# Kernel tuning notes

Hardware: AMD Instinct MI355X
Metric: run time of the kernel (lower is better)

## Reference

```python
import jax, jax.numpy as jnp
import numpy as np

N_ENT = 40000
N_REL2 = 500      # num_rel * 2
E_DIR = 200000
E_2HOP = 50000
D_IN = 128        # entity/relation init dim
D_EMB = 256       # embed_dim
N_HEADS = 4
N_HID = D_EMB // N_HEADS  # 64
LRELU_ALPHA = 0.2
BN_EPS = 1e-5


def setup_inputs() -> dict:
    key = jax.random.key(0)
    ks = jax.random.split(key, 13)
    s = 0.1  # weight init scale
    return {
        "edge_index": jax.random.randint(ks[0], (2, E_DIR), 0, N_ENT),
        "edge_type": jax.random.randint(ks[1], (E_DIR,), 0, N_REL2),
        "indices_2hop": jax.random.randint(ks[2], (E_2HOP, 4), 0, N_REL2),
        "init_embed": jax.random.normal(ks[3], (N_ENT, D_IN), jnp.float32) * s,
        "init_rel": jax.random.normal(ks[4], (N_REL2, D_IN), jnp.float32) * s,
        "W_heads": jax.random.normal(ks[5], (N_HEADS, 2 * D_IN + D_IN, N_HID), jnp.float32) * s,
        "a_heads": jax.random.normal(ks[6], (N_HEADS, N_HID, 1), jnp.float32) * s,
        "gat_W": jax.random.normal(ks[7], (D_IN, D_EMB), jnp.float32) * s,
        "out_W": jax.random.normal(ks[8], (2 * D_EMB + D_EMB, D_EMB), jnp.float32) * s,
        "out_a": jax.random.normal(ks[9], (D_EMB, 1), jnp.float32) * s,
        "W_entities": jax.random.normal(ks[10], (D_IN, D_EMB), jnp.float32) * s,
        "bn_gamma": jnp.ones((D_EMB,), jnp.float32),
        "bn_beta": jnp.zeros((D_EMB,), jnp.float32),
    }


def segment_softmax(logits, idx, num_seg):
    # sparse softmax grouped by idx (PyG-style): subtract per-segment max, exp, normalize
    m = jax.ops.segment_max(logits, idx, num_segments=num_seg)
    e = jnp.exp(logits - m[idx])
    s = jax.ops.segment_sum(e, idx, num_segments=num_seg)
    return e / (s[idx] + 1e-16)


def reference(edge_index, edge_type, indices_2hop, init_embed, init_rel,
              W_heads, a_heads, gat_W, out_W, out_a, W_entities, bn_gamma, bn_beta):
    n = init_embed.shape[0]
    # build full edge list: flipped direct edges + 2-hop edges
    edge_nhop = jnp.stack([indices_2hop[:, 3], indices_2hop[:, 0]])  # [2, E2]
    ei = jnp.concatenate([edge_index[::-1], edge_nhop], axis=1)      # [2, Etot]
    row, col = ei[0], ei[1]
    t0, t1 = indices_2hop[:, 1], indices_2hop[:, 2]

    # first-layer edge relation embeddings
    edge_embed = jnp.concatenate([init_rel[edge_type], init_rel[t0] + init_rel[t1]], axis=0)
    feat = jnp.concatenate([init_embed[row], init_embed[col], edge_embed], axis=1)  # [Etot, 3*D_IN]

    def head(W, a):
        eh = feat @ W                                     # [Etot, N_HID]
        logit = jax.nn.leaky_relu((eh @ a)[:, 0], LRELU_ALPHA)
        alpha = segment_softmax(logit, row, n)
        agg = jax.ops.segment_sum(alpha[:, None] * eh, row, num_segments=n)
        return jax.nn.elu(agg)                            # concat=True -> elu

    x = jax.vmap(head)(W_heads, a_heads)                  # [H, N, N_HID]
    x = jnp.transpose(x, (1, 0, 2)).reshape(n, -1)        # [N, H*N_HID]

    r = init_rel @ gat_W                                  # [R2, D_EMB]
    edge_embed2 = jnp.concatenate([r[edge_type], r[t0] + r[t1]], axis=0)
    feat2 = jnp.concatenate([x[row], x[col], edge_embed2], axis=1)  # [Etot, 3*D_EMB]
    eh2 = feat2 @ out_W                                   # [Etot, D_EMB]
    logit2 = jax.nn.leaky_relu((eh2 @ out_a)[:, 0], LRELU_ALPHA)
    alpha2 = segment_softmax(logit2, row, n)
    out = jax.ops.segment_sum(alpha2[:, None] * eh2, row, num_segments=n)
    x = jax.nn.elu(out)                                   # elu applied in GAT.forward

    x = x + init_embed @ W_entities
    # BatchNorm1d (training-mode batch stats, biased variance)
    mu = jnp.mean(x, axis=0)
    var = jnp.var(x, axis=0)
    x = (x - mu) / jnp.sqrt(var + BN_EPS) * bn_gamma + bn_beta
    return x, r
```

## Files before the change

kernel.cpp:

```cpp
#include <hip/hip_runtime.h>
#include <hip/hip_bf16.h>
#include <math.h>

#define N_ENT 40000
#define N_REL 500
#define E_DIR 200000
#define E_2HOP 50000
#define E_TOT 250000
#define D_IN 128
#define D_EMB 256
#define LRELU 0.2f
#define BN_EPS 1e-5f
#define NB_SCAN 157
#define NB_EDGE 977
#define N_HEAVY 500
#define DEG_SPLIT 32

typedef __hip_bfloat16 bf16;
typedef __attribute__((ext_vector_type(8))) short short8;
typedef __attribute__((ext_vector_type(4))) float float4v;

__device__ __forceinline__ float b2f(bf16 v){ return __bfloat162float(v); }
__device__ __forceinline__ float bitsf(unsigned int u){ return __builtin_bit_cast(float, u); }
__device__ __forceinline__ unsigned short bbits(float v){ return __builtin_bit_cast(unsigned short, __float2bfloat16(v)); }

__device__ __forceinline__ int e_row(int e, const int* ei, const int* i2){
  return (e < E_DIR) ? ei[E_DIR + e] : i2[(e - E_DIR)*4 + 3];
}

__global__ void prep_hist(const float* __restrict__ Wh, const float* __restrict__ ow,
                          const float* __restrict__ we, const float* __restrict__ emb,
                          bf16* __restrict__ WAp, bf16* __restrict__ WBp, bf16* __restrict__ WEp,
                          bf16* __restrict__ OWp0, bf16* __restrict__ OWp1, float* __restrict__ WC,
                          bf16* __restrict__ embb,
                          const int* __restrict__ ei, const int* __restrict__ i2, int* __restrict__ cnt){
  const int HS = 384*64;
  int b = blockIdx.x, tid = threadIdx.x;
  if (b < NB_EDGE){
    int e = b*256 + tid;
    if (e < E_TOT) atomicAdd(&cnt[e_row(e, ei, i2)], 1);
    return;
  }
  b -= NB_EDGE;
  if (b >= 240){
    int i = (b - 240)*256 + tid;
    embb[i] = __float2bfloat16(emb[i]);
    return;
  }
  if (b < 112){
    int seg, base;
    if      (b < 16){ seg = 0; base = 0; }
    else if (b < 32){ seg = 1; base = 16; }
    else if (b < 48){ seg = 2; base = 32; }
    else if (b < 80){ seg = 3; base = 48; }
    else            { seg = 4; base = 80; }
    int idx = (b - base)*256 + tid;
    int lane = idx & 63, nt = (idx >> 6) & 15, kc = idx >> 10;
    int quad = lane >> 4, l16 = lane & 15;
    int col = nt*16 + l16;
    int kbase = kc*32 + quad*8;
    bf16* dst = (seg==0?WAp : seg==1?WBp : seg==2?WEp : seg==3?OWp0 : OWp1) + (size_t)idx*8;
    #pragma unroll
    for (int j = 0; j < 8; j++){
      int k = kbase + j;
      float v;
      if      (seg == 0) v = Wh[(col>>6)*HS + k*64 + (col&63)];
      else if (seg == 1) v = Wh[(col>>6)*HS + (k+128)*64 + (col&63)];
      else if (seg == 2) v = we[(size_t)k*256 + col];
      else if (seg == 3) v = ow[(size_t)k*256 + col];
      else               v = ow[(size_t)(k+256)*256 + col];
      dst[j] = __float2bfloat16(v);
    }
  } else {
    int idx = (b - 112)*256 + tid;
    int k = idx >> 8, col = idx & 255;
    WC[idx] = Wh[(col>>6)*HS + (k+256)*64 + (col&63)];
  }
}

__global__ void scan_bsum(const int* __restrict__ cnt, int* __restrict__ bsum){
  int i = blockIdx.x*256 + threadIdx.x;
  int v = (i < N_ENT) ? cnt[i] : 0;
  int lane = threadIdx.x & 63, w = threadIdx.x >> 6;
  int s = v;
  #pragma unroll
  for (int o = 32; o >= 1; o >>= 1) s += __shfl_xor(s, o, 64);
  __shared__ int ws[4];
  if (lane == 0) ws[w] = s;
  __syncthreads();
  if (threadIdx.x == 0) bsum[blockIdx.x] = ws[0]+ws[1]+ws[2]+ws[3];
}

__global__ __launch_bounds__(256) void scan_final2(const int* __restrict__ cnt,
    const int* __restrict__ bsum, int* __restrict__ off){
  __shared__ int boffs[NB_SCAN];
  __shared__ int ws4[4];
  __shared__ int ws2[4];
  __shared__ int totals;
  int t = threadIdx.x;
  int lane = t & 63, w = t >> 6;
  {
    int v = (t < NB_SCAN) ? bsum[t] : 0;
    int s = v;
    #pragma unroll
    for (int o = 1; o < 64; o <<= 1){ int n = __shfl_up(s, o, 64); if (lane >= o) s += n; }
    if (lane == 63) ws4[w] = s;
    __syncthreads();
    int add = 0;
    for (int k = 0; k < w; k++) add += ws4[k];
    int incl = s + add;
    if (t < NB_SCAN) boffs[t] = incl - v;
    if (t == NB_SCAN-1) totals = incl;
  }
  __syncthreads();
  int i = blockIdx.x*256 + t;
  int v = (i < N_ENT) ? cnt[i] : 0;
  int s = v;
  #pragma unroll
  for (int o = 1; o < 64; o <<= 1){ int n = __shfl_up(s, o, 64); if (lane >= o) s += n; }
  if (lane == 63) ws2[w] = s;
  __syncthreads();
  int add = boffs[blockIdx.x];
  for (int k = 0; k < w; k++) add += ws2[k];
  if (i < N_ENT) off[i] = add + s - v;
  if (blockIdx.x == 0 && t == 0) off[N_ENT] = totals;
}

__device__ __forceinline__ void mfma_panel(const short* __restrict__ A,
    const short* __restrict__ Bp, bf16* __restrict__ C, int K,
    const float* __restrict__ avec, float* __restrict__ Sout, int dmode, int bx){
  int w = threadIdx.x >> 6, lane = threadIdx.x & 63;
  int quad = lane >> 4, l16 = lane & 15;
  int rm = bx*64 + w*16;
  int arow = rm + l16;
  float4v acc[16];
  #pragma unroll
  for (int nt = 0; nt < 16; nt++) acc[nt] = (float4v){0.f,0.f,0.f,0.f};
  int nkc = K >> 5;
  const short8* Ap = (const short8*)(A + (size_t)arow*K);
  const short8* Bv = (const short8*)Bp;
  short8 a_cur = Ap[quad];
  for (int kc = 0; kc < nkc; kc++){
    int kn = (kc + 1 < nkc) ? kc + 1 : kc;
    short8 a_nxt = Ap[kn*4 + quad];
    const short8* bp = Bv + (size_t)kc*16*64 + lane;
    short8 b[8];
    #pragma unroll
    for (int nt = 0; nt < 8; nt++) b[nt] = bp[(size_t)nt*64];
    #pragma unroll
    for (int nt = 0; nt < 8; nt++)
      acc[nt] = __builtin_amdgcn_mfma_f32_16x16x32_bf16(a_cur, b[nt], acc[nt], 0, 0, 0);
    #pragma unroll
    for (int nt = 0; nt < 8; nt++) b[nt] = bp[(size_t)(nt+8)*64];
    #pragma unroll
    for (int nt = 0; nt < 8; nt++)
      acc[nt+8] = __builtin_amdgcn_mfma_f32_16x16x32_bf16(a_cur, b[nt], acc[nt+8], 0, 0, 0);
    a_cur = a_nxt;
  }
  #pragma unroll
  for (int nt = 0; nt < 16; nt++){
    #pragma unroll
    for (int r = 0; r < 4; r++){
      int row = quad*4 + r;
      C[(size_t)(rm + row)*256 + nt*16 + l16] = __float2bfloat16(acc[nt][r]);
    }
  }
  if (Sout){
    if (dmode == 0){
      #pragma unroll
      for (int h = 0; h < 4; h++){
        float pr[4] = {0.f,0.f,0.f,0.f};
        #pragma unroll
        for (int ntl = 0; ntl < 4; ntl++){
          int nt = h*4 + ntl;
          float av = avec[nt*16 + l16];
          #pragma unroll
          for (int r = 0; r < 4; r++) pr[r] += acc[nt][r]*av;
        }
        #pragma unroll
        for (int m = 8; m >= 1; m >>= 1)
          #pragma unroll
          for (int r = 0; r < 4; r++) pr[r] += __shfl_xor(pr[r], m, 64);
        if (l16 == 0){
          #pragma unroll
          for (int r = 0; r < 4; r++) Sout[(rm + quad*4 + r)*4 + h] = pr[r];
        }
      }
    } else {
      float pr[4] = {0.f,0.f,0.f,0.f};
      #pragma unroll
      for (int nt = 0; nt < 16; nt++){
        float av = avec[nt*16 + l16];
        #pragma unroll
        for (int r = 0; r < 4; r++) pr[r] += acc[nt][r]*av;
      }
      #pragma unroll
      for (int m = 8; m >= 1; m >>= 1)
        #pragma unroll
        for (int r = 0; r < 4; r++) pr[r] += __shfl_xor(pr[r], m, 64);
      if (l16 == 0){
        #pragma unroll
        for (int r = 0; r < 4; r++) Sout[rm + quad*4 + r] = pr[r];
      }
    }
  }
}

__device__ __forceinline__ void gemm64_body(const float* __restrict__ A,
    const float* __restrict__ B, float* __restrict__ C, bf16* __restrict__ Cb,
    int M, int K, const float* __restrict__ av, float* __restrict__ So, int mode,
    int bxx, int byy){
  const int N = 256;
  __shared__ float As[16][65];
  __shared__ float Bs[16][65];
  int bm = bxx * 64, bn = byy * 64;
  int tid = threadIdx.x;
  int tx = tid & 15, ty = tid >> 4;
  float acc[4][4] = {};
  for (int k0 = 0; k0 < K; k0 += 16){
    #pragma unroll
    for (int j = 0; j < 4; j++){
      int idx = tid + j*256;
      int m = idx >> 4, kk = idx & 15;
      int gm = bm + m;
      float v = 0.f;
      if (gm < M) v = A[(size_t)gm*K + k0 + kk];
      As[kk][m] = v;
    }
    #pragma unroll
    for (int j = 0; j < 4; j++){
      int idx = tid + j*256;
      int kk = idx >> 6, n = idx & 63;
      Bs[kk][n] = B[(size_t)(k0+kk)*N + bn + n];
    }
    __syncthreads();
    #pragma unroll
    for (int kk = 0; kk < 16; kk++){
      float a[4], b[4];
      #pragma unroll
      for (int i = 0; i < 4; i++) a[i] = As[kk][ty*4+i];
      #pragma unroll
      for (int j = 0; j < 4; j++) b[j] = Bs[kk][tx*4+j];
      #pragma unroll
      for (int i = 0; i < 4; i++)
        #pragma unroll
        for (int j = 0; j < 4; j++) acc[i][j] += a[i]*b[j];
    }
    __syncthreads();
  }
  if (Cb){
    #pragma unroll
    for (int i = 0; i < 4; i++){
      int gm = bm + ty*4 + i;
      if (gm >= M) continue;
      #pragma unroll
      for (int j = 0; j < 4; j++)
        Cb[(size_t)gm*N + bn + tx*4 + j] = __float2bfloat16(acc[i][j]);
    }
  } else {
    #pragma unroll
    for (int i = 0; i < 4; i++){
      int gm = bm + ty*4 + i;
      if (gm >= M) continue;
      #pragma unroll
      for (int j = 0; j < 4; j++)
        C[(size_t)gm*N + bn + tx*4 + j] = acc[i][j];
    }
  }
  if (mode != 2){
    float pr[4];
    #pragma unroll
    for (int i = 0; i < 4; i++){
      float p = 0.f;
      #pragma unroll
      for (int j = 0; j < 4; j++) p += acc[i][j]*av[bn + tx*4 + j];
      pr[i] = p;
    }
    #pragma unroll
    for (int m = 8; m >= 1; m >>= 1)
      #pragma unroll
      for (int i = 0; i < 4; i++) pr[i] += __shfl_xor(pr[i], m, 64);
    if (tx == 0){
      #pragma unroll
      for (int i = 0; i < 4; i++){
        int gm = bm + ty*4 + i;
        if (gm < M){
          if (mode == 0) So[gm*4 + byy] = pr[i];
          else atomicAdd(&So[gm], pr[i]);
        }
      }
    }
  }
}

__device__ __forceinline__ void scatter_body(const int* __restrict__ ei, const int* __restrict__ et,
    const int* __restrict__ i2, const int* __restrict__ off,
    int* __restrict__ cur, int4* __restrict__ EIDX, int blk){
  int e = blk*256 + threadIdx.x;
  if (e >= E_TOT) return;
  int r = e_row(e, ei, i2);
  int p = atomicAdd(&cur[r], 1);
  int d = off[r] + p;
  int4 v;
  if (e < E_DIR){ v.x = ei[e]; v.y = et[e]; v.z = -1; }
  else { int q = (e - E_DIR)*4; v.x = i2[q]; v.y = i2[q+1]; v.z = i2[q+2]; }
  v.w = r;
  EIDX[d] = v;
}

__global__ __launch_bounds__(256) void mega1(
    const short* __restrict__ embb, const short* __restrict__ WAp, const short* __restrict__ WBp,
    const short* __restrict__ WEp, bf16* __restrict__ P1, bf16* __restrict__ P2, bf16* __restrict__ EP,
    const float* __restrict__ ah, float* __restrict__ S1, float* __restrict__ S2,
    const float* __restrict__ rel, const float* __restrict__ WC, const float* __restrict__ gw,
    float* __restrict__ RF, float* __restrict__ SRm, bf16* __restrict__ PRb,
    const int* __restrict__ ei, const int* __restrict__ et, const int* __restrict__ i2,
    const int* __restrict__ off, int* __restrict__ cur, int4* __restrict__ EIDX, int useEP){
  int y = blockIdx.y, x = blockIdx.x;
  if (x < 625){
    if (y == 2 && !useEP) return;
    const short* B = y==0 ? WAp : (y==1 ? WBp : WEp);
    bf16* C = y==0 ? P1 : (y==1 ? P2 : EP);
    float* S = y==0 ? S1 : (y==1 ? S2 : nullptr);
    mfma_panel(embb, B, C, 128, ah, S, 0, x);
    return;
  }
  int r = x - 625;
  if (y == 0){
    if (r < 64){
      int z = r >> 5, rr = r & 31, by = rr >> 3, bx = rr & 7;
      if (z == 0) gemm64_body(rel, WC, nullptr, PRb, N_REL, 128, ah, SRm, 0, bx, by);
      else        gemm64_body(rel, gw, RF, nullptr, N_REL, 128, nullptr, nullptr, 2, bx, by);
    }
  } else if (y == 1){
    if (r < NB_EDGE) scatter_body(ei, et, i2, off, cur, EIDX, r);
  }
}

__global__ __launch_bounds__(256) void mega2(
    const short* __restrict__ X1s, const short* __restrict__ OWp0, const short* __restrict__ OWp1,
    bf16* __restrict__ Q1, bf16* __restrict__ Q2, const float* __restrict__ oa,
    float* __restrict__ S1B, float* __restrict__ S2B,
    const float* __restrict__ RF, const float* __restrict__ owB, float* __restrict__ SRB,
    bf16* __restrict__ QRb){
  int y = blockIdx.y, x = blockIdx.x;
  if (x < 625){
    mfma_panel(X1s, y==0 ? OWp0 : OWp1, y==0 ? Q1 : Q2, 256, oa, y==0 ? S1B : S2B, 1, x);
    return;
  }
  int r = x - 625;
  if (y == 0 && r < 32){
    int by = r >> 3, bx = r & 7;
    gemm64_body(RF, owB, nullptr, QRb, N_REL, 256, oa, SRB, 1, bx, by);
  }
}

__global__ void gemm64_acc(const float* __restrict__ A, const float* __restrict__ B,
                           float* __restrict__ C, int M, int K){
  const int N = 256;
  __shared__ float As[16][65];
  __shared__ float Bs[16][65];
  int bm = blockIdx.x * 64, bn = blockIdx.y * 64;
  int tid = threadIdx.x;
  int tx = tid & 15, ty = tid >> 4;
  float acc[4][4] = {};
  for (int k0 = 0; k0 < K; k0 += 16){
    #pragma unroll
    for (int j = 0; j < 4; j++){
      int idx = tid + j*256;
      int m = idx >> 4, kk = idx & 15;
      int gm = bm + m;
      float v = 0.f;
      if (gm < M) v = A[(size_t)gm*K + k0 + kk];
      As[kk][m] = v;
    }
    #pragma unroll
    for (int j = 0; j < 4; j++){
      int idx = tid + j*256;
      int kk = idx >> 6, n = idx & 63;
      Bs[kk][n] = B[(size_t)(k0+kk)*N + bn + n];
    }
    __syncthreads();
    #pragma unroll
    for (int kk = 0; kk < 16; kk++){
      float a[4], b[4];
      #pragma unroll
      for (int i = 0; i < 4; i++) a[i] = As[kk][ty*4+i];
      #pragma unroll
      for (int j = 0; j < 4; j++) b[j] = Bs[kk][tx*4+j];
      #pragma unroll
      for (int i = 0; i < 4; i++)
        #pragma unroll
        for (int j = 0; j < 4; j++) acc[i][j] += a[i]*b[j];
    }
    __syncthreads();
  }
  #pragma unroll
  for (int i = 0; i < 4; i++){
    int gm = bm + ty*4 + i;
    if (gm >= M) continue;
    #pragma unroll
    for (int j = 0; j < 4; j++){
      size_t o = (size_t)gm*N + bn + tx*4 + j;
      C[o] += acc[i][j];
    }
  }
}

__global__ __launch_bounds__(256) void sm1f(const int* __restrict__ off, const int4* __restrict__ EIDX,
    const float* __restrict__ s1, const float* __restrict__ s2, const float* __restrict__ sR,
    float* __restrict__ L1, float* __restrict__ AS1, float* __restrict__ IV1){
  if (blockIdx.x < N_HEAVY){
    int i = blockIdx.x;
    int st = off[i], en = off[i+1];
    if (en - st <= DEG_SPLIT) return;
    int h = threadIdx.x >> 6, lane = threadIdx.x & 63;
    float* Lh = L1 + (size_t)h*E_TOT;
    float si = s1[i*4 + h];
    float mx = -1e30f;
    for (int t = st + lane; t < en; t += 64){
      int4 e = EIDX[t];
      float v = si + s2[e.x*4+h] + sR[e.y*4+h];
      if (e.z >= 0) v += sR[e.z*4+h];
      v = (v >= 0.f) ? v : LRELU*v;
      Lh[t] = v;
      mx = fmaxf(mx, v);
    }
    #pragma unroll
    for (int o = 32; o >= 1; o >>= 1) mx = fmaxf(mx, __shfl_xor(mx, o, 64));
    float sm = 0.f;
    for (int t = st + lane; t < en; t += 64){
      float ev = __expf(Lh[t] - mx); Lh[t] = ev; sm += ev;
    }
    #pragma unroll
    for (int o = 32; o >= 1; o >>= 1) sm += __shfl_xor(sm, o, 64);
    float inv = 1.f/(sm + 1e-16f);
    if (lane == 0){ AS1[i*4+h] = sm*inv; IV1[i*4+h] = inv; }
    return;
  }
  int wid = threadIdx.x >> 6, lane = threadIdx.x & 63;
  int i = (blockIdx.x - N_HEAVY)*4 + wid;
  if (i >= N_ENT) return;
  int st = off[i], en = off[i+1];
  if (i < N_HEAVY && en - st > DEG_SPLIT) return;
  int hf = lane >> 4, l16 = lane & 15;
  float* Lh = L1 + (size_t)hf*E_TOT;
  float si = s1[i*4 + hf];
  if (en - st > 2*16){
    float mx = -1e30f;
    for (int t = st + l16; t < en; t += 16){
      int4 e = EIDX[t];
      float v = si + s2[e.x*4+hf] + sR[e.y*4+hf];
      if (e.z >= 0) v += sR[e.z*4+hf];
      v = (v >= 0.f) ? v : LRELU*v;
      Lh[t] = v; mx = fmaxf(mx, v);
    }
    #pragma unroll
    for (int o = 8; o >= 1; o >>= 1) mx = fmaxf(mx, __shfl_xor(mx, o, 64));
    float sm = 0.f;
    for (int t = st + l16; t < en; t += 16){
      float ev = __expf(Lh[t] - mx); Lh[t] = ev; sm += ev;
    }
    #pragma unroll
    for (int o = 8; o >= 1; o >>= 1) sm += __shfl_xor(sm, o, 64);
    float inv = 1.f/(sm + 1e-16f);
    if (l16 == 0){ AS1[i*4+hf] = sm*inv; IV1[i*4+hf] = inv; }
    return;
  }
  int t0 = st + l16, t1 = t0 + 16;
  float v0 = -1e30f, v1 = -1e30f;
  if (t0 < en){
    int4 e = EIDX[t0];
    float v = si + s2[e.x*4+hf] + sR[e.y*4+hf];
    if (e.z >= 0) v += sR[e.z*4+hf];
    v0 = (v >= 0.f) ? v : LRELU*v;
  }
  if (t1 < en){
    int4 e = EIDX[t1];
    float v = si + s2[e.x*4+hf] + sR[e.y*4+hf];
    if (e.z >= 0) v += sR[e.z*4+hf];
    v1 = (v >= 0.f) ? v : LRELU*v;
  }
  float mx = fmaxf(v0, v1);
  #pragma unroll
  for (int o = 8; o >= 1; o >>= 1) mx = fmaxf(mx, __shfl_xor(mx, o, 64));
  float sm = 0.f;
  if (t0 < en){ float ev = __expf(v0 - mx); Lh[t0] = ev; sm += ev; }
  if (t1 < en){ float ev = __expf(v1 - mx); Lh[t1] = ev; sm += ev; }
  #pragma unroll
  for (int o = 8; o >= 1; o >>= 1) sm += __shfl_xor(sm, o, 64);
  float inv = 1.f/(sm + 1e-16f);
  if (l16 == 0){ AS1[i*4+hf] = sm*inv; IV1[i*4+hf] = inv; }
}

__global__ __launch_bounds__(256) void sm2f(const int* __restrict__ off, const int4* __restrict__ EIDX,
    const float* __restrict__ s1, const float* __restrict__ s2, const float* __restrict__ sR,
    float* __restrict__ L2, float* __restrict__ AS2, float* __restrict__ IV2){
  __shared__ float wsm[4], wss[4];
  if (blockIdx.x < N_HEAVY){
    int i = blockIdx.x;
    int st = off[i], en = off[i+1];
    if (en - st <= DEG_SPLIT) return;
    int tid = threadIdx.x, w = tid >> 6, lane = tid & 63;
    float si = s1[i];
    float mx = -1e30f;
    for (int t = st + tid; t < en; t += 256){
// ... 321 lines not shown
  }
  float a0=0,a1=0,a2=0,a3=0;
  int t = st;
  int n4 = st + ((en - st) & ~3);
  for (; t < n4; t += 4){
    int4 e[4]; float wv[4]; uint2 u[4]; uint2 rr[4];
    #pragma unroll
    for (int k = 0; k < 4; k++){ e[k] = EIDX[t+k]; wv[k] = W2[t+k]; }
    #pragma unroll
    for (int k = 0; k < 4; k++){
      u[k] = *(const uint2*)(Q2 + (size_t)e[k].x*256 + f0);
      rr[k] = *(const uint2*)(QRm + (size_t)e[k].y*256 + f0);
    }
    float rf[4][4];
    #pragma unroll
    for (int k = 0; k < 4; k++){ UNPK(rr[k], rf[k][0], rf[k][1], rf[k][2], rf[k][3]) }
    #pragma unroll
    for (int k = 0; k < 4; k++){
      if (e[k].z >= 0){
        uint2 s = *(const uint2*)(QRm + (size_t)e[k].z*256 + f0);
        float s0,s1,s2,s3; UNPK(s, s0,s1,s2,s3)
        rf[k][0] += s0; rf[k][1] += s1; rf[k][2] += s2; rf[k][3] += s3;
      }
    }
    #pragma unroll
    for (int k = 0; k < 4; k++){
      a0 += wv[k]*(bitsf(u[k].x << 16) + rf[k][0]);
      a1 += wv[k]*(bitsf(u[k].x & 0xffff0000u) + rf[k][1]);
      a2 += wv[k]*(bitsf(u[k].y << 16) + rf[k][2]);
      a3 += wv[k]*(bitsf(u[k].y & 0xffff0000u) + rf[k][3]);
    }
  }
  for (; t < en; t++){
    float w = W2[t];
    int4 e = EIDX[t];
    uint2 u = *(const uint2*)(Q2 + (size_t)e.x*256 + f0);
    uint2 rr = *(const uint2*)(QRm + (size_t)e.y*256 + f0);
    float r0,r1,r2,r3; UNPK(rr, r0,r1,r2,r3)
    if (e.z >= 0){
      uint2 s = *(const uint2*)(QRm + (size_t)e.z*256 + f0);
      float s0,s1,s2,s3; UNPK(s, s0,s1,s2,s3)
      r0 += s0; r1 += s1; r2 += s2; r3 += s3;
    }
    a0 += w*(bitsf(u.x << 16) + r0);
    a1 += w*(bitsf(u.x & 0xffff0000u) + r1);
    a2 += w*(bitsf(u.y << 16) + r2);
    a3 += w*(bitsf(u.y & 0xffff0000u) + r3);
  }
  float iv = IV2[i];
  a0 *= iv; a1 *= iv; a2 *= iv; a3 *= iv;
  float as = AS2[i];
  uint2 uq = *(const uint2*)(Q1 + ob);
  a0 += as*bitsf(uq.x << 16);
  a1 += as*bitsf(uq.x & 0xffff0000u);
  a2 += as*bitsf(uq.y << 16);
  a3 += as*bitsf(uq.y & 0xffff0000u);
  a0 = ((a0 > 0.f) ? a0 : __expf(a0)-1.f) + ep0;
  a1 = ((a1 > 0.f) ? a1 : __expf(a1)-1.f) + ep1;
  a2 = ((a2 > 0.f) ? a2 : __expf(a2)-1.f) + ep2;
  a3 = ((a3 > 0.f) ? a3 : __expf(a3)-1.f) + ep3;
  *(float4*)(X2 + ob) = (float4){a0, a1, a2, a3};
}

__global__ void bn_reduce(const float* __restrict__ X, float* __restrict__ sums, float* __restrict__ sq){
  int ch = threadIdx.x;
  float s = 0.f, q = 0.f;
  for (int r = blockIdx.x; r < N_ENT; r += gridDim.x){
    float v = X[(size_t)r*256 + ch];
    s += v; q += v*v;
  }
  atomicAdd(&sums[ch], s);
  atomicAdd(&sq[ch], q);
}

__global__ void bn_final_r(float* __restrict__ X, const float* __restrict__ sums, const float* __restrict__ sq,
                           const float* __restrict__ gamma, const float* __restrict__ beta,
                           const float* __restrict__ RF, float* __restrict__ out_r){
  int b = blockIdx.x;
  if (b < 40000){
    int idx = b*256 + threadIdx.x;
    int ch = idx & 255;
    const float invn = 1.f/(float)N_ENT;
    float mean = sums[ch] * invn;
    float var  = fmaxf(sq[ch] * invn - mean*mean, 0.f);
    X[idx] = (X[idx] - mean) * rsqrtf(var + BN_EPS) * gamma[ch] + beta[ch];
  } else {
    int idx = (b - 40000)*256 + threadIdx.x;
    out_r[idx] = RF[idx];
  }
}

extern "C" void kernel_launch(void* const* d_in, const int* in_sizes, int n_in,
                              void* d_out, int out_size, void* d_ws, size_t ws_size,
                              hipStream_t stream){
  const int*   ei  = (const int*)d_in[0];
  const int*   et  = (const int*)d_in[1];
  const int*   i2  = (const int*)d_in[2];
  const float* emb = (const float*)d_in[3];
  const float* rel = (const float*)d_in[4];
  const float* Wh  = (const float*)d_in[5];
  const float* ah  = (const float*)d_in[6];
  const float* gw  = (const float*)d_in[7];
  const float* ow  = (const float*)d_in[8];
  const float* oa  = (const float*)d_in[9];
  const float* we  = (const float*)d_in[10];
  const float* gma = (const float*)d_in[11];
  const float* bta = (const float*)d_in[12];
  float* out = (float*)d_out;

  char* ws = (char*)d_ws;
  size_t o = 0;
  auto alloc = [&](size_t bytes)->char*{
    char* p = ws + o; o = (o + bytes + 255) & ~(size_t)255; return p;
  };
  bf16*  P1  = (bf16*)alloc(20480000);
  bf16*  P2  = (bf16*)alloc(20480000);
  bf16*  PRb = (bf16*)alloc(256000);
  bf16*  QRb = (bf16*)alloc(256000);
  float* RF  = (float*)alloc(512000);
  float* WC  = (float*)alloc(131072);
  bf16*  WAp = (bf16*)alloc(65536);
  bf16*  WBp = (bf16*)alloc(65536);
  bf16*  WEp = (bf16*)alloc(65536);
  bf16*  OWp0= (bf16*)alloc(131072);
  bf16*  OWp1= (bf16*)alloc(131072);
  float* S1  = (float*)alloc(640000);
  float* S2  = (float*)alloc(640000);
  float* SRm = (float*)alloc(8192);
  float* S1B = (float*)alloc(160000);
  float* S2B = (float*)alloc(160000);
  int*   CNT = (int*)alloc(160000);
  int*   CUR = (int*)alloc(160000);
  float* SRB = (float*)alloc(2048);
  float* BNS = (float*)alloc(1024);
  float* BNQ = (float*)alloc(1024);
  int*   OFF = (int*)alloc(160016);
  int*   BSUM= (int*)alloc(1024);
  int4*  EIDX= (int4*)alloc(4000000);
  float* L1  = (float*)alloc(4000000);
  float* L2  = (float*)alloc(1000000);
  float* AS1 = (float*)alloc(640000);
  float* AS2 = (float*)alloc(160000);
  float* IV1 = (float*)alloc(640000);
  float* IV2 = (float*)alloc(160000);
  size_t base_end = o;
  bool useEP = (ws_size >= base_end + 20480256 + 512);
  bf16* EP = nullptr;
  if (useEP) EP = (bf16*)alloc(20480000);
  bf16* X1b  = (bf16*)out;
  bf16* embb = (bf16*)((char*)out + 20480000);
  float* X2 = out;
  (void)in_sizes; (void)n_in; (void)out_size;

  hipMemsetAsync(CNT, 0, 324096, stream);

  prep_hist<<<NB_EDGE + 20240, 256, 0, stream>>>(Wh, ow, we, emb,
      WAp, WBp, WEp, OWp0, OWp1, WC, embb, ei, i2, CNT);

  scan_bsum<<<NB_SCAN, 256, 0, stream>>>(CNT, BSUM);
  scan_final2<<<NB_SCAN, 256, 0, stream>>>(CNT, BSUM, OFF);

  mega1<<<dim3(625 + NB_EDGE, 3), 256, 0, stream>>>(
      (const short*)embb, (const short*)WAp, (const short*)WBp, (const short*)WEp,
      P1, P2, EP, ah, S1, S2,
      rel, WC, gw, RF, SRm, PRb,
      ei, et, i2, OFF, CUR, EIDX, useEP ? 1 : 0);

  sm1f<<<N_HEAVY + N_ENT/4, 256, 0, stream>>>(OFF, EIDX, S1, S2, SRm, L1, AS1, IV1);
  agg1<<<N_HEAVY + N_ENT/4, 256, 0, stream>>>(OFF, EIDX, L1, AS1, IV1, P1, P2, PRb, X1b);

  mega2<<<dim3(625 + 32, 2), 256, 0, stream>>>(
      (const short*)X1b, (const short*)OWp0, (const short*)OWp1,
      P1, P2, oa, S1B, S2B, RF, ow + 131072, SRB, QRb);

  sm2f<<<N_HEAVY + N_ENT/4, 256, 0, stream>>>(OFF, EIDX, S1B, S2B, SRB, L2, AS2, IV2);
  agg2<<<N_HEAVY + N_ENT/4, 256, 0, stream>>>(OFF, EIDX, L2, AS2, IV2, P1, P2, QRb, EP, X2);

  if (!useEP)
    gemm64_acc<<<dim3((N_ENT+63)/64, 4), 256, 0, stream>>>(emb, we, X2, N_ENT, 128);

  bn_reduce<<<1024, 256, 0, stream>>>(X2, BNS, BNQ);
  bn_final_r<<<40500, 256, 0, stream>>>(X2, BNS, BNQ, gma, bta, RF, out + (size_t)N_ENT*256);
}
```

Before: 404.6 us.

## Split MFMA panels into column halves with atomic score accumulation

Each MFMA panel block now computes only half of the 256 output columns, so there are twice as many blocks and half as many accumulator registers per thread, with launch bounds raised to allow more waves per CU. The per-row attention dot products in the second layer are now combined across the two halves with atomicAdd, which requires zeroing the score buffers; the memset is widened to start at S1B. Shared memory is moved to an explicit buffer so the combined kernels use one allocation. The aim is better occupancy and latency hiding in the projection GEMMs, at the cost of reloading A rows twice and adding atomics.

```diff
diff --git a/kernel.cpp b/kernel.cpp
--- a/kernel.cpp
+++ b/kernel.cpp
@@ -128,54 +128,54 @@
 
 __device__ __forceinline__ void mfma_panel(const short* __restrict__ A,
     const short* __restrict__ Bp, bf16* __restrict__ C, int K,
-    const float* __restrict__ avec, float* __restrict__ Sout, int dmode, int bx){
+    const float* __restrict__ avec, float* __restrict__ Sout, int dmode,
+    int bx, int half){
   int w = threadIdx.x >> 6, lane = threadIdx.x & 63;
   int quad = lane >> 4, l16 = lane & 15;
   int rm = bx*64 + w*16;
   int arow = rm + l16;
-  float4v acc[16];
+  float4v acc[8];
   #pragma unroll
-  for (int nt = 0; nt < 16; nt++) acc[nt] = (float4v){0.f,0.f,0.f,0.f};
+  for (int nt = 0; nt < 8; nt++) acc[nt] = (float4v){0.f,0.f,0.f,0.f};
   int nkc = K >> 5;
   const short8* Ap = (const short8*)(A + (size_t)arow*K);
-  const short8* Bv = (const short8*)Bp;
+  const short8* Bv = (const short8*)Bp + half*512 + lane;
   short8 a_cur = Ap[quad];
   for (int kc = 0; kc < nkc; kc++){
     int kn = (kc + 1 < nkc) ? kc + 1 : kc;
     short8 a_nxt = Ap[kn*4 + quad];
-    const short8* bp = Bv + (size_t)kc*16*64 + lane;
-    short8 b[8];
-    #pragma unroll
-    for (int nt = 0; nt < 8; nt++) b[nt] = bp[(size_t)nt*64];
-    #pragma unroll
-    for (int nt = 0; nt < 8; nt++)
+    const short8* bp = Bv + (size_t)kc*1024;
+    short8 b[4];
+    #pragma unroll
+    for (int nt = 0; nt < 4; nt++) b[nt] = bp[nt*64];
+    #pragma unroll
+    for (int nt = 0; nt < 4; nt++)
       acc[nt] = __builtin_amdgcn_mfma_f32_16x16x32_bf16(a_cur, b[nt], acc[nt], 0, 0, 0);
     #pragma unroll
-    for (int nt = 0; nt < 8; nt++) b[nt] = bp[(size_t)(nt+8)*64];
-    #pragma unroll
-    for (int nt = 0; nt < 8; nt++)
-      acc[nt+8] = __builtin_amdgcn_mfma_f32_16x16x32_bf16(a_cur, b[nt], acc[nt+8], 0, 0, 0);
+    for (int nt = 0; nt < 4; nt++) b[nt] = bp[(nt+4)*64];
+    #pragma unroll
+    for (int nt = 0; nt < 4; nt++)
+      acc[nt+4] = __builtin_amdgcn_mfma_f32_16x16x32_bf16(a_cur, b[nt], acc[nt+4], 0, 0, 0);
     a_cur = a_nxt;
   }
   #pragma unroll
-  for (int nt = 0; nt < 16; nt++){
-    #pragma unroll
-    for (int r = 0; r < 4; r++){
-      int row = quad*4 + r;
-      C[(size_t)(rm + row)*256 + nt*16 + l16] = __float2bfloat16(acc[nt][r]);
-    }
+  for (int nt = 0; nt < 8; nt++){
+    int col = (half*8 + nt)*16 + l16;
+    #pragma unroll
+    for (int r = 0; r < 4; r++)
+      C[(size_t)(rm + quad*4 + r)*256 + col] = __float2bfloat16(acc[nt][r]);
   }
   if (Sout){
     if (dmode == 0){
       #pragma unroll
-      for (int h = 0; h < 4; h++){
+      for (int hl = 0; hl < 2; hl++){
         float pr[4] = {0.f,0.f,0.f,0.f};
         #pragma unroll
         for (int ntl = 0; ntl < 4; ntl++){
-          int nt = h*4 + ntl;
-          float av = avec[nt*16 + l16];
+          int ln = hl*4 + ntl;
+          float av = avec[(half*8 + ln)*16 + l16];
           #pragma unroll
-          for (int r = 0; r < 4; r++) pr[r] += acc[nt][r]*av;
+          for (int r = 0; r < 4; r++) pr[r] += acc[ln][r]*av;
         }
         #pragma unroll
         for (int m = 8; m >= 1; m >>= 1)
@@ -183,16 +183,17 @@
           for (int r = 0; r < 4; r++) pr[r] += __shfl_xor(pr[r], m, 64);
         if (l16 == 0){
           #pragma unroll
-          for (int r = 0; r < 4; r++) Sout[(rm + quad*4 + r)*4 + h] = pr[r];
+          for (int r = 0; r < 4; r++)
+            Sout[(rm + quad*4 + r)*4 + half*2 + hl] = pr[r];
         }
       }
     } else {
       float pr[4] = {0.f,0.f,0.f,0.f};
       #pragma unroll
-      for (int nt = 0; nt < 16; nt++){
-        float av = avec[nt*16 + l16];
+      for (int ln = 0; ln < 8; ln++){
+        float av = avec[(half*8 + ln)*16 + l16];
         #pragma unroll
-        for (int r = 0; r < 4; r++) pr[r] += acc[nt][r]*av;
+        for (int r = 0; r < 4; r++) pr[r] += acc[ln][r]*av;
       }
       #pragma unroll
       for (int m = 8; m >= 1; m >>= 1)
@@ -200,7 +201,7 @@
         for (int r = 0; r < 4; r++) pr[r] += __shfl_xor(pr[r], m, 64);
       if (l16 == 0){
         #pragma unroll
-        for (int r = 0; r < 4; r++) Sout[rm + quad*4 + r] = pr[r];
+        for (int r = 0; r < 4; r++) atomicAdd(&Sout[rm + quad*4 + r], pr[r]);
       }
     }
   }
@@ -209,10 +210,10 @@
 __device__ __forceinline__ void gemm64_body(const float* __restrict__ A,
     const float* __restrict__ B, float* __restrict__ C, bf16* __restrict__ Cb,
     int M, int K, const float* __restrict__ av, float* __restrict__ So, int mode,
-    int bxx, int byy){
+    int bxx, int byy, char* smem){
   const int N = 256;
-  __shared__ float As[16][65];
-  __shared__ float Bs[16][65];
+  float (*As)[65] = (float (*)[65])smem;
+  float (*Bsf)[65] = (float (*)[65])(smem + 16*65*sizeof(float));
   int bm = bxx * 64, bn = byy * 64;
   int tid = threadIdx.x;
   int tx = tid & 15, ty = tid >> 4;
@@ -231,7 +232,7 @@
     for (int j = 0; j < 4; j++){
       int idx = tid + j*256;
       int kk = idx >> 6, n = idx & 63;
-      Bs[kk][n] = B[(size_t)(k0+kk)*N + bn + n];
+      Bsf[kk][n] = B[(size_t)(k0+kk)*N + bn + n];
     }
     __syncthreads();
     #pragma unroll
@@ -240,7 +241,7 @@
       #pragma unroll
       for (int i = 0; i < 4; i++) a[i] = As[kk][ty*4+i];
       #pragma unroll
-      for (int j = 0; j < 4; j++) b[j] = Bs[kk][tx*4+j];
+      for (int j = 0; j < 4; j++) b[j] = Bsf[kk][tx*4+j];
       #pragma unroll
       for (int i = 0; i < 4; i++)
         #pragma unroll
@@ -308,7 +309,7 @@
   EIDX[d] = v;
 }
 
-__global__ __launch_bounds__(256) void mega1(
+__global__ __launch_bounds__(256, 4) void mega1(
     const short* __restrict__ embb, const short* __restrict__ WAp, const short* __restrict__ WBp,
     const short* __restrict__ WEp, bf16* __restrict__ P1, bf16* __restrict__ P2, bf16* __restrict__ EP,
     const float* __restrict__ ah, float* __restrict__ S1, float* __restrict__ S2,
@@ -316,42 +317,45 @@
     float* __restrict__ RF, float* __restrict__ SRm, bf16* __restrict__ PRb,
     const int* __restrict__ ei, const int* __restrict__ et, const int* __restrict__ i2,
     const int* __restrict__ off, int* __restrict__ cur, int4* __restrict__ EIDX, int useEP){
+  __shared__ char smem[8704];
   int y = blockIdx.y, x = blockIdx.x;
-  if (x < 625){
+  if (x < 1250){
     if (y == 2 && !useEP) return;
     const short* B = y==0 ? WAp : (y==1 ? WBp : WEp);
     bf16* C = y==0 ? P1 : (y==1 ? P2 : EP);
     float* S = y==0 ? S1 : (y==1 ? S2 : nullptr);
-    mfma_panel(embb, B, C, 128, ah, S, 0, x);
-    return;
-  }
-  int r = x - 625;
+    mfma_panel(embb, B, C, 128, ah, S, 0, x >> 1, x & 1);
+    return;
+  }
+  int r = x - 1250;
   if (y == 0){
     if (r < 64){
       int z = r >> 5, rr = r & 31, by = rr >> 3, bx = rr & 7;
-      if (z == 0) gemm64_body(rel, WC, nullptr, PRb, N_REL, 128, ah, SRm, 0, bx, by);
-      else        gemm64_body(rel, gw, RF, nullptr, N_REL, 128, nullptr, nullptr, 2, bx, by);
+      if (z == 0) gemm64_body(rel, WC, nullptr, PRb, N_REL, 128, ah, SRm, 0, bx, by, smem);
+      else        gemm64_body(rel, gw, RF, nullptr, N_REL, 128, nullptr, nullptr, 2, bx, by, smem);
     }
   } else if (y == 1){
     if (r < NB_EDGE) scatter_body(ei, et, i2, off, cur, EIDX, r);
   }
 }
 
-__global__ __launch_bounds__(256) void mega2(
+__global__ __launch_bounds__(256, 4) void mega2(
     const short* __restrict__ X1s, const short* __restrict__ OWp0, const short* __restrict__ OWp1,
     bf16* __restrict__ Q1, bf16* __restrict__ Q2, const float* __restrict__ oa,
     float* __restrict__ S1B, float* __restrict__ S2B,
     const float* __restrict__ RF, const float* __restrict__ owB, float* __restrict__ SRB,
     bf16* __restrict__ QRb){
+  __shared__ char smem[8704];
   int y = blockIdx.y, x = blockIdx.x;
-  if (x < 625){
-    mfma_panel(X1s, y==0 ? OWp0 : OWp1, y==0 ? Q1 : Q2, 256, oa, y==0 ? S1B : S2B, 1, x);
-    return;
-  }
-  int r = x - 625;
+  if (x < 1250){
+    mfma_panel(X1s, y==0 ? OWp0 : OWp1, y==0 ? Q1 : Q2, 256, oa,
+               y==0 ? S1B : S2B, 1, x >> 1, x & 1);
+    return;
+  }
+  int r = x - 1250;
   if (y == 0 && r < 32){
     int by = r >> 3, bx = r & 7;
-    gemm64_body(RF, owB, nullptr, QRb, N_REL, 256, oa, SRB, 1, bx, by);
+    gemm64_body(RF, owB, nullptr, QRb, N_REL, 256, oa, SRB, 1, bx, by, smem);
   }
 }
 
@@ -979,7 +983,7 @@
   float* X2 = out;
   (void)in_sizes; (void)n_in; (void)out_size;
 
-  hipMemsetAsync(CNT, 0, 324096, stream);
+  hipMemsetAsync(S1B, 0, 644096, stream);
 
   prep_hist<<<NB_EDGE + 20240, 256, 0, stream>>>(Wh, ow, we, emb,
       WAp, WBp, WEp, OWp0, OWp1, WC, embb, ei, i2, CNT);
@@ -987,7 +991,7 @@
   scan_bsum<<<NB_SCAN, 256, 0, stream>>>(CNT, BSUM);
   scan_final2<<<NB_SCAN, 256, 0, stream>>>(CNT, BSUM, OFF);
 
-  mega1<<<dim3(625 + NB_EDGE, 3), 256, 0, stream>>>(
+  mega1<<<dim3(1250 + NB_EDGE, 3), 256, 0, stream>>>(
       (const short*)embb, (const short*)WAp, (const short*)WBp, (const short*)WEp,
       P1, P2, EP, ah, S1, S2,
       rel, WC, gw, RF, SRm, PRb,
@@ -996,7 +1000,7 @@
   sm1f<<<N_HEAVY + N_ENT/4, 256, 0, stream>>>(OFF, EIDX, S1, S2, SRm, L1, AS1, IV1);
   agg1<<<N_HEAVY + N_ENT/4, 256, 0, stream>>>(OFF, EIDX, L1, AS1, IV1, P1, P2, PRb, X1b);
 
-  mega2<<<dim3(625 + 32, 2), 256, 0, stream>>>(
+  mega2<<<dim3(1250 + 32, 2), 256, 0, stream>>>(
       (const short*)X1b, (const short*)OWp0, (const short*)OWp1,
       P1, P2, oa, S1B, S2B, RF, ow + 131072, SRB, QRb);
 
```

Result: no change. 401.3 us (-0.8%).

## Stage MFMA panel output through LDS and interleave panel tiles for A reuse

Applied to the files above, without the earlier changes.

The MFMA panel routine now loads the whole A row strip into registers up front with a compile-time K. It writes results to shared memory and then emits coalesced 16-byte stores, replacing scattered 2-byte bf16 stores. The 2D grids are flattened, and tiles are ordered so the projections sharing the same A tile run in neighbouring blocks, which should improve L2 reuse. The cost is 33KB of static LDS per block plus a barrier, which may lower occupancy, and more registers from the preloaded A fragments.

```diff
diff --git a/kernel.cpp b/kernel.cpp
--- a/kernel.cpp
+++ b/kernel.cpp
@@ -15,6 +15,8 @@
 #define NB_EDGE 977
 #define N_HEAVY 500
 #define DEG_SPLIT 32
+#define G1 1896
+#define G2 1264
 
 typedef __hip_bfloat16 bf16;
 typedef __attribute__((ext_vector_type(8))) short short8;
@@ -126,44 +128,37 @@
   if (blockIdx.x == 0 && t == 0) off[N_ENT] = totals;
 }
 
-__device__ __forceinline__ void mfma_panel(const short* __restrict__ A,
-    const short* __restrict__ Bp, bf16* __restrict__ C, int K,
-    const float* __restrict__ avec, float* __restrict__ Sout, int dmode, int bx){
-  int w = threadIdx.x >> 6, lane = threadIdx.x & 63;
+template<int NKC>
+__device__ __forceinline__ void mfma_panel2(const short* __restrict__ A,
+    const short* __restrict__ Bp, bf16* __restrict__ C,
+    const float* __restrict__ avec, float* __restrict__ Sout, int dmode,
+    int tile, char* smem){
+  int tid = threadIdx.x, w = tid >> 6, lane = tid & 63;
   int quad = lane >> 4, l16 = lane & 15;
-  int rm = bx*64 + w*16;
+  int rm = tile*64 + w*16;
   int arow = rm + l16;
+  const short8* Ap = (const short8*)(A + (size_t)arow*(NKC*32));
+  short8 a[NKC];
+  #pragma unroll
+  for (int kc = 0; kc < NKC; kc++) a[kc] = Ap[kc*4 + quad];
   float4v acc[16];
   #pragma unroll
   for (int nt = 0; nt < 16; nt++) acc[nt] = (float4v){0.f,0.f,0.f,0.f};
-  int nkc = K >> 5;
-  const short8* Ap = (const short8*)(A + (size_t)arow*K);
-  const short8* Bv = (const short8*)Bp;
-  short8 a_cur = Ap[quad];
-  for (int kc = 0; kc < nkc; kc++){
-    int kn = (kc + 1 < nkc) ? kc + 1 : kc;
-    short8 a_nxt = Ap[kn*4 + quad];
-    const short8* bp = Bv + (size_t)kc*16*64 + lane;
+  const short8* Bv = (const short8*)Bp + lane;
+  #pragma unroll
+  for (int kc = 0; kc < NKC; kc++){
+    const short8* bp = Bv + (size_t)kc*1024;
     short8 b[8];
     #pragma unroll
-    for (int nt = 0; nt < 8; nt++) b[nt] = bp[(size_t)nt*64];
+    for (int nt = 0; nt < 8; nt++) b[nt] = bp[nt*64];
     #pragma unroll
     for (int nt = 0; nt < 8; nt++)
-      acc[nt] = __builtin_amdgcn_mfma_f32_16x16x32_bf16(a_cur, b[nt], acc[nt], 0, 0, 0);
-    #pragma unroll
-    for (int nt = 0; nt < 8; nt++) b[nt] = bp[(size_t)(nt+8)*64];
+      acc[nt] = __builtin_amdgcn_mfma_f32_16x16x32_bf16(a[kc], b[nt], acc[nt], 0, 0, 0);
+    #pragma unroll
+    for (int nt = 0; nt < 8; nt++) b[nt] = bp[(nt+8)*64];
     #pragma unroll
     for (int nt = 0; nt < 8; nt++)
-      acc[nt+8] = __builtin_amdgcn_mfma_f32_16x16x32_bf16(a_cur, b[nt], acc[nt+8], 0, 0, 0);
-    a_cur = a_nxt;
-  }
-  #pragma unroll
-  for (int nt = 0; nt < 16; nt++){
-    #pragma unroll
-    for (int r = 0; r < 4; r++){
-      int row = quad*4 + r;
-      C[(size_t)(rm + row)*256 + nt*16 + l16] = __float2bfloat16(acc[nt][r]);
-    }
+      acc[nt+8] = __builtin_amdgcn_mfma_f32_16x16x32_bf16(a[kc], b[nt], acc[nt+8], 0, 0, 0);
   }
   if (Sout){
     if (dmode == 0){
@@ -204,15 +199,29 @@
       }
     }
   }
+  bf16* Cs = (bf16*)smem;
+  #pragma unroll
+  for (int nt = 0; nt < 16; nt++){
+    #pragma unroll
+    for (int r = 0; r < 4; r++)
+      Cs[(w*16 + quad*4 + r)*260 + nt*16 + l16] = __float2bfloat16(acc[nt][r]);
+  }
+  __syncthreads();
+  int row = tid >> 2, c4 = tid & 3;
+  const char* Lr = smem + row*520;
+  float4* Cr = (float4*)(C + (size_t)(tile*64 + row)*256);
+  #pragma unroll
+  for (int j = 0; j < 8; j++)
+    Cr[c4 + j*4] = *(const float4*)(Lr + (c4 + j*4)*16);
 }
 
 __device__ __forceinline__ void gemm64_body(const float* __restrict__ A,
     const float* __restrict__ B, float* __restrict__ C, bf16* __restrict__ Cb,
     int M, int K, const float* __restrict__ av, float* __restrict__ So, int mode,
-    int bxx, int byy){
+    int bxx, int byy, char* smem){
   const int N = 256;
-  __shared__ float As[16][65];
-  __shared__ float Bs[16][65];
+  float (*As)[65] = (float (*)[65])smem;
+  float (*Bsf)[65] = (float (*)[65])(smem + 16*65*sizeof(float));
   int bm = bxx * 64, bn = byy * 64;
   int tid = threadIdx.x;
   int tx = tid & 15, ty = tid >> 4;
@@ -231,7 +240,7 @@
     for (int j = 0; j < 4; j++){
       int idx = tid + j*256;
       int kk = idx >> 6, n = idx & 63;
-      Bs[kk][n] = B[(size_t)(k0+kk)*N + bn + n];
+      Bsf[kk][n] = B[(size_t)(k0+kk)*N + bn + n];
     }
     __syncthreads();
     #pragma unroll
@@ -240,7 +249,7 @@
       #pragma unroll
       for (int i = 0; i < 4; i++) a[i] = As[kk][ty*4+i];
       #pragma unroll
-      for (int j = 0; j < 4; j++) b[j] = Bs[kk][tx*4+j];
+      for (int j = 0; j < 4; j++) b[j] = Bsf[kk][tx*4+j];
       #pragma unroll
       for (int i = 0; i < 4; i++)
         #pragma unroll
@@ -316,25 +325,28 @@
     float* __restrict__ RF, float* __restrict__ SRm, bf16* __restrict__ PRb,
     const int* __restrict__ ei, const int* __restrict__ et, const int* __restrict__ i2,
     const int* __restrict__ off, int* __restrict__ cur, int4* __restrict__ EIDX, int useEP){
-  int y = blockIdx.y, x = blockIdx.x;
-  if (x < 625){
-    if (y == 2 && !useEP) return;
-    const short* B = y==0 ? WAp : (y==1 ? WBp : WEp);
-    bf16* C = y==0 ? P1 : (y==1 ? P2 : EP);
-    float* S = y==0 ? S1 : (y==1 ? S2 : nullptr);
-    mfma_panel(embb, B, C, 128, ah, S, 0, x);
-    return;
-  }
-  int r = x - 625;
-  if (y == 0){
-    if (r < 64){
-      int z = r >> 5, rr = r & 31, by = rr >> 3, bx = rr & 7;
-      if (z == 0) gemm64_body(rel, WC, nullptr, PRb, N_REL, 128, ah, SRm, 0, bx, by);
-      else        gemm64_body(rel, gw, RF, nullptr, N_REL, 128, nullptr, nullptr, 2, bx, by);
-    }
-  } else if (y == 1){
-    if (r < NB_EDGE) scatter_body(ei, et, i2, off, cur, EIDX, r);
-  }
+  __shared__ char smem[33280];
+  int x = blockIdx.x;
+  if (x < G1){
+    int grp = x / 24, sub = x % 24;
+    int tile = grp*8 + (sub & 7), p = sub >> 3;
+    if (tile >= 625) return;
+    if (p == 2 && !useEP) return;
+    const short* B = p==0 ? WAp : (p==1 ? WBp : WEp);
+    bf16* C = p==0 ? P1 : (p==1 ? P2 : EP);
+    float* S = p==0 ? S1 : (p==1 ? S2 : nullptr);
+    mfma_panel2<4>(embb, B, C, ah, S, 0, tile, smem);
+    return;
+  }
+  int r = x - G1;
+  if (r < 64){
+    int z = r >> 5, rr = r & 31, by = rr >> 3, bx = rr & 7;
+    if (z == 0) gemm64_body(rel, WC, nullptr, PRb, N_REL, 128, ah, SRm, 0, bx, by, smem);
+    else        gemm64_body(rel, gw, RF, nullptr, N_REL, 128, nullptr, nullptr, 2, bx, by, smem);
+    return;
+  }
+  r -= 64;
+  if (r < NB_EDGE) scatter_body(ei, et, i2, off, cur, EIDX, r);
 }
 
 __global__ __launch_bounds__(256) void mega2(
@@ -343,15 +355,20 @@
     float* __restrict__ S1B, float* __restrict__ S2B,
     const float* __restrict__ RF, const float* __restrict__ owB, float* __restrict__ SRB,
     bf16* __restrict__ QRb){
-  int y = blockIdx.y, x = blockIdx.x;
-  if (x < 625){
-    mfma_panel(X1s, y==0 ? OWp0 : OWp1, y==0 ? Q1 : Q2, 256, oa, y==0 ? S1B : S2B, 1, x);
-    return;
-  }
-  int r = x - 625;
-  if (y == 0 && r < 32){
+  __shared__ char smem[33280];
+  int x = blockIdx.x;
+  if (x < G2){
+    int grp = x / 16, sub = x % 16;
+    int tile = grp*8 + (sub & 7), p = sub >> 3;
+    if (tile >= 625) return;
+    mfma_panel2<8>(X1s, p==0 ? OWp0 : OWp1, p==0 ? Q1 : Q2, oa,
+                   p==0 ? S1B : S2B, 1, tile, smem);
+    return;
+  }
+  int r = x - G2;
+  if (r < 32){
     int by = r >> 3, bx = r & 7;
-    gemm64_body(RF, owB, nullptr, QRb, N_REL, 256, oa, SRB, 1, bx, by);
+    gemm64_body(RF, owB, nullptr, QRb, N_REL, 256, oa, SRB, 1, bx, by, smem);
   }
 }
 
@@ -987,7 +1004,7 @@
   scan_bsum<<<NB_SCAN, 256, 0, stream>>>(CNT, BSUM);
   scan_final2<<<NB_SCAN, 256, 0, stream>>>(CNT, BSUM, OFF);
 
-  mega1<<<dim3(625 + NB_EDGE, 3), 256, 0, stream>>>(
+  mega1<<<G1 + 64 + NB_EDGE, 256, 0, stream>>>(
       (const short*)embb, (const short*)WAp, (const short*)WBp, (const short*)WEp,
       P1, P2, EP, ah, S1, S2,
       rel, WC, gw, RF, SRm, PRb,
@@ -996,7 +1013,7 @@
   sm1f<<<N_HEAVY + N_ENT/4, 256, 0, stream>>>(OFF, EIDX, S1, S2, SRm, L1, AS1, IV1);
   agg1<<<N_HEAVY + N_ENT/4, 256, 0, stream>>>(OFF, EIDX, L1, AS1, IV1, P1, P2, PRb, X1b);
 
-  mega2<<<dim3(625 + 32, 2), 256, 0, stream>>>(
+  mega2<<<G2 + 32, 256, 0, stream>>>(
       (const short*)X1b, (const short*)OWp0, (const short*)OWp1,
       P1, P2, oa, S1B, S2B, RF, ow + 131072, SRB, QRb);
 
```

New measurement: 405.8 us. About the same (+0.3%).
